# Performance work log

Measured on AMD Instinct MI355X. Metric: run time of the kernel, lower is better.

The kernel has to match this reference:

```python
import jax, jax.numpy as jnp
import numpy as np

N_EV, N_OBJ, D = 50000, 100000, 256
E1, E2 = 400000, 800000


def _ln(x, g, b):
    m = x.mean(-1, keepdims=True)
    v = x.var(-1, keepdims=True)
    return (x - m) * jax.lax.rsqrt(v + 1e-5) * g + b


def _lrelu(x):
    return jax.nn.leaky_relu(x, 0.2)


def setup_inputs():
    key = jax.random.key(0)
    ks = jax.random.split(key, 24)
    s = 1.0 / np.sqrt(D)
    W = lambda i, shp: (jax.random.normal(ks[i], shp, jnp.float32) * s)
    inp = {
        'object_X': jax.random.normal(ks[0], (N_OBJ, D), jnp.float32),
        'event_X': jax.random.normal(ks[1], (N_EV, D), jnp.float32),
        'Wo': W(2, (D, D)), 'bo': jnp.zeros((D,), jnp.float32),
        'go': jnp.ones((D,), jnp.float32), 'bon': jnp.zeros((D,), jnp.float32),
        'We': W(3, (D, D)), 'be': jnp.zeros((D,), jnp.float32),
        'ge': jnp.ones((D,), jnp.float32), 'ben': jnp.zeros((D,), jnp.float32),
        'Wu': W(4, (D, D)), 'bu': jnp.zeros((D,), jnp.float32),
        'Wl': W(5, (D, D)), 'bl': jnp.zeros((D,), jnp.float32),
        'g1': jnp.ones((D,), jnp.float32), 'b1': jnp.zeros((D,), jnp.float32),
        'g2': jnp.ones((D,), jnp.float32), 'b2': jnp.zeros((D,), jnp.float32),
        'Wh1': W(6, (D, D)), 'ah1': W(7, (2 * D,)),
        'Wh2': W(8, (D, D)), 'ah2': W(9, (2 * D,)),
        'oe_ev': jax.random.randint(ks[10], (E1,), 0, N_EV, jnp.int32),
        'oe_obj': jax.random.randint(ks[11], (E1,), 0, N_OBJ, jnp.int32),
        'hg_node': jax.random.randint(ks[12], (E2,), 0, N_EV + N_OBJ, jnp.int32),
        'hg_edge': jax.random.randint(ks[13], (E2,), 0, N_EV, jnp.int32),
        'total_events': N_EV,
    }
    return inp


def reference(object_X, event_X, Wo, bo, go, bon, We, be, ge, ben,
              Wu, bu, Wl, bl, g1, b1, g2, b2, Wh1, ah1, Wh2, ah2,
              oe_ev, oe_obj, hg_node, hg_edge, total_events):
    # proj chains (Dropout is identity at eval)
    obj = _ln(_lrelu(object_X @ Wo + bo), go, bon)
    ev = _ln(_lrelu(event_X @ We + be), ge, ben)
    # ObjectStateUpdater: aggregate incident-event features per object, project
    msg = jax.ops.segment_sum(ev[oe_ev], oe_obj, num_segments=N_OBJ)
    obj1 = _ln(_lrelu(msg @ Wu + bu) + obj, g1, b1)
    # LifecycleStateUpdater: linear lifecycle state transition
    obj2 = _ln(_lrelu(obj1 @ Wl + bl) + obj1, g2, b2)
    X = jnp.concatenate([ev, obj2], axis=0)  # [N_EV+N_OBJ, D]
    n_nodes = N_EV + N_OBJ

    def hgnn(X, W, a):
        m = (X @ W)[hg_node]  # [E2, D] gathered node messages
        cnt = jax.ops.segment_sum(jnp.ones((E2,), X.dtype), hg_edge, num_segments=total_events)
        ef = jax.ops.segment_sum(m, hg_edge, num_segments=total_events) / jnp.maximum(cnt, 1.0)[:, None]
        gth = ef[hg_edge]  # [E2, D] hyperedge feature per incidence
        score = _lrelu(m @ a[:D] + gth @ a[D:])  # [E2]
        smax = jax.ops.segment_max(score, hg_node, num_segments=n_nodes)
        e = jnp.exp(score - smax[hg_node])
        z = jax.ops.segment_sum(e, hg_node, num_segments=n_nodes)
        attn = e / jnp.maximum(z, 1e-9)[hg_node]
        out = jax.ops.segment_sum(attn[:, None] * gth, hg_node, num_segments=n_nodes)
        return _lrelu(out), attn

    h, _ = hgnn(X, Wh1, ah1)
    h, attn = hgnn(h, Wh2, ah2)  # layer-2 attention is what get_attention_weights() returns
    return (h, attn)
```

## Files before the change

### kernel.cpp

```cpp
#include <hip/hip_runtime.h>
#include <cstdio>

typedef __attribute__((ext_vector_type(8))) short short8_t;
typedef __attribute__((ext_vector_type(8))) unsigned short ushort8_t;
typedef __attribute__((ext_vector_type(4))) unsigned short us4;
typedef __attribute__((ext_vector_type(4))) float f32x4;

__device__ __forceinline__ unsigned short f2bf(float f) {
  unsigned u = __float_as_uint(f);
  u = u + 0x7FFFu + ((u >> 16) & 1u);
  return (unsigned short)(u >> 16);
}
__device__ __forceinline__ float bf2f(unsigned short h) {
  return __uint_as_float((unsigned)h << 16);
}
__device__ __forceinline__ float lrelu(float x) { return x > 0.f ? x : 0.2f * x; }


__global__ void k_transpose_w6(const float* __restrict__ W0, const float* __restrict__ W1,
                               const float* __restrict__ W2, const float* __restrict__ W3,
                               const float* __restrict__ W4, const float* __restrict__ W5,
                               unsigned short* __restrict__ WT) {
  int which = blockIdx.x >> 8, k = blockIdx.x & 255, n = threadIdx.x;
  const float* W = which == 0 ? W0 : which == 1 ? W1 : which == 2 ? W2
                 : which == 3 ? W3 : which == 4 ? W4 : W5;
  WT[(size_t)which * 65536 + n * 256 + k] = f2bf(W[k * 256 + n]);
}


__global__ void k_count3(const int* __restrict__ hg_node, const int* __restrict__ hg_edge,
                         const int* __restrict__ oe_obj, int* __restrict__ cn,
                         int* __restrict__ ce, int* __restrict__ co, int nE2, int nE1) {
  int e = blockIdx.x * blockDim.x + threadIdx.x;
  if (e < nE2) {
    atomicAdd(&cn[hg_node[e]], 1);
    atomicAdd(&ce[hg_edge[e]], 1);
  }
  if (e < nE1) atomicAdd(&co[oe_obj[e]], 1);
}

__global__ void k_fill3(const int* __restrict__ hg_node, const int* __restrict__ hg_edge,
                        const int* __restrict__ oe_ev, const int* __restrict__ oe_obj,
                        const int* __restrict__ NS, const int* __restrict__ ES,
                        const int* __restrict__ OS, int* __restrict__ curn,
                        int* __restrict__ cure, int* __restrict__ curo,
                        int2* __restrict__ PE, int* __restrict__ NDe, int* __restrict__ EVo,
                        int nE2, int nE1) {
  int e = blockIdx.x * blockDim.x + threadIdx.x;
  if (e < nE2) {
    int sn = hg_node[e], se = hg_edge[e];
    int pn = NS[sn] + atomicAdd(&curn[sn], 1);
    PE[pn] = make_int2(e, se);
    int pe = ES[se] + atomicAdd(&cure[se], 1);
    NDe[pe] = sn;
  }
  if (e < nE1) {
    int so = oe_obj[e];
    int po = OS[so] + atomicAdd(&curo[so], 1);
    EVo[po] = oe_ev[e];
  }
}

__global__ __launch_bounds__(1024) void k_scan3(const int* __restrict__ c0, int* __restrict__ s0,
                                                int n0, const int* __restrict__ c1,
                                                int* __restrict__ s1, int n1,
                                                const int* __restrict__ c2, int* __restrict__ s2,
                                                int n2) {
  const int* cnt;
  int* starts;
  int n;
  if (blockIdx.x == 0) { cnt = c0; starts = s0; n = n0; }
  else if (blockIdx.x == 1) { cnt = c1; starts = s1; n = n1; }
  else { cnt = c2; starts = s2; n = n2; }
  __shared__ int wsum[16];
  int tid = threadIdx.x, lane = tid & 63, w = tid >> 6;
  int carry = 0;
  for (int base = 0; base < n; base += 4096) {
    int i0 = base + tid * 4;
    int4 c = make_int4(0, 0, 0, 0);
    if (i0 + 3 < n) c = *(const int4*)(cnt + i0);
    else {
      if (i0 < n) c.x = cnt[i0];
      if (i0 + 1 < n) c.y = cnt[i0 + 1];
      if (i0 + 2 < n) c.z = cnt[i0 + 2];
      if (i0 + 3 < n) c.w = cnt[i0 + 3];
    }
    int tsum = c.x + c.y + c.z + c.w;
    int inc = tsum;
    for (int o = 1; o < 64; o <<= 1) {
      int v = __shfl_up(inc, o);
      if (lane >= o) inc += v;
    }
    if (lane == 63) wsum[w] = inc;
    __syncthreads();
    int woff = 0;
    for (int k = 0; k < w; k++) woff += wsum[k];
    int excl = carry + woff + inc - tsum;
    if (i0 < n) starts[i0] = excl;
    if (i0 + 1 < n) starts[i0 + 1] = excl + c.x;
    if (i0 + 2 < n) starts[i0 + 2] = excl + c.x + c.y;
    if (i0 + 3 < n) starts[i0 + 3] = excl + c.x + c.y + c.z;
    int total = 0;
    for (int k = 0; k < 16; k++) total += wsum[k];
    carry += total;
    __syncthreads();
  }
  if (tid == 0) starts[n] = carry;
}

template <int HAS_SKIP, int A_F32>
__global__ __launch_bounds__(256) void k_gemm_ln(const void* __restrict__ Av,
                                                 const unsigned short* __restrict__ Bt,
                                                 const float* __restrict__ bias,
                                                 const float* __restrict__ gamma,
                                                 const float* __restrict__ beta,
                                                 const unsigned short* skip,
                                                 unsigned short* outb, int rows) {
  __shared__ unsigned short As[64][40];
  __shared__ unsigned short Bs[256][40];
  int tid = threadIdx.x;
  int wave = tid >> 6, lane = tid & 63;
  int quad = lane >> 4, l16 = lane & 15;
  size_t row0 = (size_t)blockIdx.x * 64;

  f32x4 acc[16];
#pragma unroll
  for (int i = 0; i < 16; i++) acc[i] = (f32x4){0.f, 0.f, 0.f, 0.f};

  int ar = tid >> 2, ac = (tid & 3) * 8;
  size_t arow = row0 + ar;
  for (int k0 = 0; k0 < 256; k0 += 32) {
    if (A_F32) {
      float4 f0 = make_float4(0.f, 0.f, 0.f, 0.f), f1 = f0;
      if (arow < (size_t)rows) {
        const float4* ap = (const float4*)((const float*)Av + arow * 256 + k0 + ac);
        f0 = ap[0];
        f1 = ap[1];
      }
      us4 u0 = {f2bf(f0.x), f2bf(f0.y), f2bf(f0.z), f2bf(f0.w)};
      us4 u1 = {f2bf(f1.x), f2bf(f1.y), f2bf(f1.z), f2bf(f1.w)};
      *(us4*)&As[ar][ac] = u0;
      *(us4*)&As[ar][ac + 4] = u1;
    } else {
      *(ushort8_t*)&As[ar][ac] =
          *(const ushort8_t*)&((const unsigned short*)Av)[arow * 256 + k0 + ac];
    }
    const unsigned short* bp = &Bt[(size_t)tid * 256 + k0];
    *(ushort8_t*)&Bs[tid][0] = *(const ushort8_t*)&bp[0];
    *(ushort8_t*)&Bs[tid][8] = *(const ushort8_t*)&bp[8];
    *(ushort8_t*)&Bs[tid][16] = *(const ushort8_t*)&bp[16];
    *(ushort8_t*)&Bs[tid][24] = *(const ushort8_t*)&bp[24];
    __syncthreads();
    short8_t afrag = *(const short8_t*)&As[wave * 16 + l16][quad * 8];
#pragma unroll
    for (int nt = 0; nt < 16; nt++) {
      short8_t bfrag = *(const short8_t*)&Bs[nt * 16 + l16][quad * 8];
      acc[nt] = __builtin_amdgcn_mfma_f32_16x16x32_bf16(afrag, bfrag, acc[nt], 0, 0, 0);
    }
    __syncthreads();
  }

  size_t rbase = row0 + wave * 16 + quad * 4;
#pragma unroll
  for (int nt = 0; nt < 16; nt++) {
    int col = nt * 16 + l16;
    float bv = bias[col];
#pragma unroll
    for (int r = 0; r < 4; r++) {
      float x = lrelu(acc[nt][r] + bv);
      if (HAS_SKIP) {
        if (rbase + r < (size_t)rows) x += bf2f(skip[(rbase + r) * 256 + col]);
      }
      acc[nt][r] = x;
    }
  }
  float s[4] = {0, 0, 0, 0}, q[4] = {0, 0, 0, 0};
#pragma unroll
  for (int nt = 0; nt < 16; nt++)
#pragma unroll
    for (int r = 0; r < 4; r++) {
      float x = acc[nt][r];
      s[r] += x;
      q[r] += x * x;
    }
#pragma unroll
  for (int o = 1; o < 16; o <<= 1)
#pragma unroll
    for (int r = 0; r < 4; r++) {
      s[r] += __shfl_xor(s[r], o);
      q[r] += __shfl_xor(q[r], o);
    }
  float mr[4], rs[4];
#pragma unroll
  for (int r = 0; r < 4; r++) {
    float m = s[r] * (1.f / 256.f);
    float v = q[r] * (1.f / 256.f) - m * m;
    mr[r] = m;
    rs[r] = rsqrtf(v + 1e-5f);
  }
#pragma unroll
  for (int nt = 0; nt < 16; nt++) {
    int col = nt * 16 + l16;
    float g = gamma[col], bb = beta[col];
#pragma unroll
    for (int r = 0; r < 4; r++) {
      if (rbase + r < (size_t)rows) {
        float y = (acc[nt][r] - mr[r]) * rs[r] * g + bb;
        outb[(rbase + r) * 256 + col] = f2bf(y);
      }
    }
  }
}

__global__ __launch_bounds__(256) void k_gemm_xw(unsigned short* A,
                                                 const unsigned short* __restrict__ Bt,
                                                 const float* __restrict__ a1,
                                                 float* __restrict__ s1, int rows) {
  __shared__ unsigned short As[64][40];
  __shared__ unsigned short Bs[256][40];
  int tid = threadIdx.x;
  int wave = tid >> 6, lane = tid & 63;
  int quad = lane >> 4, l16 = lane & 15;
  size_t row0 = (size_t)blockIdx.x * 64;

  f32x4 acc[16];
#pragma unroll
  for (int i = 0; i < 16; i++) acc[i] = (f32x4){0.f, 0.f, 0.f, 0.f};

  int ar = tid >> 2, ac = (tid & 3) * 8;
  for (int k0 = 0; k0 < 256; k0 += 32) {
    *(ushort8_t*)&As[ar][ac] = *(const ushort8_t*)&A[(row0 + ar) * 256 + k0 + ac];
    const unsigned short* bp = &Bt[(size_t)tid * 256 + k0];
    *(ushort8_t*)&Bs[tid][0] = *(const ushort8_t*)&bp[0];
    *(ushort8_t*)&Bs[tid][8] = *(const ushort8_t*)&bp[8];
    *(ushort8_t*)&Bs[tid][16] = *(const ushort8_t*)&bp[16];
    *(ushort8_t*)&Bs[tid][24] = *(const ushort8_t*)&bp[24];
    __syncthreads();
    short8_t afrag = *(const short8_t*)&As[wave * 16 + l16][quad * 8];
#pragma unroll
    for (int nt = 0; nt < 16; nt++) {
      short8_t bfrag = *(const short8_t*)&Bs[nt * 16 + l16][quad * 8];
      acc[nt] = __builtin_amdgcn_mfma_f32_16x16x32_bf16(afrag, bfrag, acc[nt], 0, 0, 0);
    }
    __syncthreads();
  }

  size_t rbase = row0 + wave * 16 + quad * 4;
  float s[4] = {0, 0, 0, 0};
#pragma unroll
  for (int nt = 0; nt < 16; nt++) {
    float av = a1[nt * 16 + l16];
#pragma unroll
    for (int r = 0; r < 4; r++) s[r] += acc[nt][r] * av;
  }
#pragma unroll
  for (int o = 1; o < 16; o <<= 1)
#pragma unroll
    for (int r = 0; r < 4; r++) s[r] += __shfl_xor(s[r], o);
#pragma unroll
  for (int nt = 0; nt < 16; nt++) {
    int col = nt * 16 + l16;
#pragma unroll
    for (int r = 0; r < 4; r++)
      if (rbase + r < (size_t)rows) A[(rbase + r) * 256 + col] = f2bf(acc[nt][r]);
  }
  if (l16 == 0) {
#pragma unroll
    for (int r = 0; r < 4; r++)
      if (rbase + r < (size_t)rows) s1[rbase + r] = s[r];
  }
}


__global__ __launch_bounds__(256) void k_edge_gather(const unsigned short* __restrict__ XW,
                                                     const int* __restrict__ ES,
                                                     const int* __restrict__ NDe,
                                                     const float* __restrict__ a2,
                                                     unsigned short* __restrict__ EF,
                                                     float* __restrict__ s2, int nEdges) {
  int wave = threadIdx.x >> 6, lane = threadIdx.x & 63;
  int r = blockIdx.x * 4 + wave;
  if (r >= nEdges) return;
  int s = ES[r], e = ES[r + 1];
  int cnt = e - s;
  float4 acc = make_float4(0.f, 0.f, 0.f, 0.f);
  if (cnt <= 64) {
    int myn = 0;
    if (lane < cnt) myn = NDe[s + lane];
    for (int base = 0; base < cnt; base += 8) {
      us4 u[8];
      float f[8];
#pragma unroll
      for (int t = 0; t < 8; t++) {
        int j2 = base + t;
        int n1 = __shfl(myn, j2);
        u[t] = ((const us4*)(XW + (size_t)n1 * 256))[lane];
        f[t] = (j2 < cnt) ? 1.f : 0.f;
      }
#pragma unroll
      for (int t = 0; t < 8; t++) {
        acc.x += f[t] * bf2f(u[t].x);
        acc.y += f[t] * bf2f(u[t].y);
        acc.z += f[t] * bf2f(u[t].z);
        acc.w += f[t] * bf2f(u[t].w);
      }
    }
  } else {
    for (int j = s; j < e; j++) {
      int n = NDe[j];
      us4 u = ((const us4*)(XW + (size_t)n * 256))[lane];
      acc.x += bf2f(u.x); acc.y += bf2f(u.y);
      acc.z += bf2f(u.z); acc.w += bf2f(u.w);
    }
  }
  float inv = 1.f / (float)(cnt > 1 ? cnt : 1);
  acc.x *= inv; acc.y *= inv; acc.z *= inv; acc.w *= inv;
  us4 ub = {f2bf(acc.x), f2bf(acc.y), f2bf(acc.z), f2bf(acc.w)};
  ((us4*)(EF + (size_t)r * 256))[lane] = ub;
  float4 a = ((const float4*)a2)[lane];
  float d = acc.x * a.x + acc.y * a.y + acc.z * a.z + acc.w * a.w;
  for (int o = 32; o; o >>= 1) d += __shfl_xor(d, o);
  if (lane == 0) s2[r] = d;
}

template <int WRITE_ATTN>
__global__ __launch_bounds__(256) void k_node_gather(const int* __restrict__ NS,
                                                     const int2* __restrict__ PE,
                                                     const float* __restrict__ s1,
                                                     const float* __restrict__ s2,
                                                     const unsigned short* __restrict__ EF,
                                                     unsigned short* outb, float* outf,
                                                     float* attn_out, int nNodes) {
  int wave = threadIdx.x >> 6, lane = threadIdx.x & 63;
  int n = blockIdx.x * 4 + wave;
  if (n >= nNodes) return;
  int s = NS[n], e = NS[n + 1];
  int cnt = e - s;
  float s1n = s1[n];
  float4 acc = make_float4(0.f, 0.f, 0.f, 0.f);
  if (cnt <= 64) {
    int mye0 = 0, myed = 0;
    float myscore = -3.4e38f;
    bool act = lane < cnt;
    if (act) {
      int2 pe = PE[s + lane];
      mye0 = pe.x;
      myed = pe.y;
      myscore = lrelu(s1n + s2[myed]);
    }
    float mymax = myscore;
    for (int o = 32; o; o >>= 1) mymax = fmaxf(mymax, __shfl_xor(mymax, o));
    float myexp = act ? __expf(myscore - mymax) : 0.f;
    float mysum = myexp;
    for (int o = 32; o; o >>= 1) mysum += __shfl_xor(mysum, o);
    float zinv = 1.f / fmaxf(mysum, 1e-9f);
    float myw = myexp * zinv;
    if (WRITE_ATTN && act) attn_out[mye0] = myw;
    for (int base = 0; base < cnt; base += 8) {
      us4 v[8];
      float w[8];
#pragma unroll
      for (int t = 0; t < 8; t++) {
        int j2 = base + t;
        int ed = __shfl(myed, j2);
        w[t] = __shfl(myw, j2);
        v[t] = ((const us4*)(EF + (size_t)ed * 256))[lane];
      }
#pragma unroll
      for (int t = 0; t < 8; t++) {
        acc.x += w[t] * bf2f(v[t].x);
        acc.y += w[t] * bf2f(v[t].y);
        acc.z += w[t] * bf2f(v[t].z);
        acc.w += w[t] * bf2f(v[t].w);
      }
    }
  } else {
    float mymax = -3.4e38f;
    for (int j = s + lane; j < e; j += 64) {
      mymax = fmaxf(mymax, lrelu(s1n + s2[PE[j].y]));
    }
    for (int o = 32; o; o >>= 1) mymax = fmaxf(mymax, __shfl_xor(mymax, o));
    float mysum = 0.f;
    for (int j = s + lane; j < e; j += 64) {
      mysum += __expf(lrelu(s1n + s2[PE[j].y]) - mymax);
    }
    for (int o = 32; o; o >>= 1) mysum += __shfl_xor(mysum, o);
    float zinv = 1.f / fmaxf(mysum, 1e-9f);
    for (int j = s; j < e; j++) {
      int2 pe = PE[j];
      float w = __expf(lrelu(s1n + s2[pe.y]) - mymax) * zinv;
      if (WRITE_ATTN) {
        if (lane == 0) attn_out[pe.x] = w;
      }
      us4 v = ((const us4*)(EF + (size_t)pe.y * 256))[lane];
      acc.x += w * bf2f(v.x); acc.y += w * bf2f(v.y);
      acc.z += w * bf2f(v.z); acc.w += w * bf2f(v.w);
    }
  }
  acc.x = lrelu(acc.x); acc.y = lrelu(acc.y);
  acc.z = lrelu(acc.z); acc.w = lrelu(acc.w);
  if (outb) {
    us4 u = {f2bf(acc.x), f2bf(acc.y), f2bf(acc.z), f2bf(acc.w)};
    ((us4*)(outb + (size_t)n * 256))[lane] = u;
  } else {
    ((float4*)(outf + (size_t)n * 256))[lane] = acc;
  }
}

__global__ __launch_bounds__(256) void k_obj_gather(const unsigned short* __restrict__ EVB,
                                                    const int* __restrict__ OS,
                                                    const int* __restrict__ EVo,
                                                    unsigned short* __restrict__ outb,
                                                    int nObj) {
  int wave = threadIdx.x >> 6, lane = threadIdx.x & 63;
  int o = blockIdx.x * 4 + wave;
  if (o >= nObj) return;
  int s = OS[o], e = OS[o + 1];
  int cnt = e - s;
  float4 acc = make_float4(0.f, 0.f, 0.f, 0.f);
  if (cnt <= 64) {
    int myev = 0;
    if (lane < cnt) myev = EVo[s + lane];
    for (int base = 0; base < cnt; base += 8) {
      us4 u[8];
      float f[8];
#pragma unroll
      for (int t = 0; t < 8; t++) {
        int j2 = base + t;
        int v1 = __shfl(myev, j2);
        u[t] = ((const us4*)(EVB + (size_t)v1 * 256))[lane];
        f[t] = (j2 < cnt) ? 1.f : 0.f;
      }
#pragma unroll
      for (int t = 0; t < 8; t++) {
        acc.x += f[t] * bf2f(u[t].x);
        acc.y += f[t] * bf2f(u[t].y);
        acc.z += f[t] * bf2f(u[t].z);
        acc.w += f[t] * bf2f(u[t].w);
      }
    }
  } else {
    for (int j = s; j < e; j++) {
      int ev = EVo[j];
      us4 u = ((const us4*)(EVB + (size_t)ev * 256))[lane];
      acc.x += bf2f(u.x); acc.y += bf2f(u.y);
      acc.z += bf2f(u.z); acc.w += bf2f(u.w);
    }
  }
  us4 u = {f2bf(acc.x), f2bf(acc.y), f2bf(acc.z), f2bf(acc.w)};
  ((us4*)(outb + (size_t)o * 256))[lane] = u;
}


extern "C" void kernel_launch(void* const* d_in, const int* in_sizes, int n_in,
                              void* d_out, int out_size, void* d_ws, size_t ws_size,
                              hipStream_t stream) {
  (void)n_in; (void)out_size;
  const float* object_X = (const float*)d_in[0];
  const float* event_X = (const float*)d_in[1];
  const float* Wo = (const float*)d_in[2];   const float* bo = (const float*)d_in[3];
  const float* go = (const float*)d_in[4];   const float* bon = (const float*)d_in[5];
  const float* We = (const float*)d_in[6];   const float* be = (const float*)d_in[7];
  const float* ge = (const float*)d_in[8];   const float* ben = (const float*)d_in[9];
  const float* Wu = (const float*)d_in[10];  const float* bu = (const float*)d_in[11];
  const float* Wl = (const float*)d_in[12];  const float* bl = (const float*)d_in[13];
  const float* g1 = (const float*)d_in[14];  const float* b1 = (const float*)d_in[15];
  const float* g2 = (const float*)d_in[16];  const float* b2 = (const float*)d_in[17];
  const float* Wh1 = (const float*)d_in[18]; const float* ah1 = (const float*)d_in[19];
  const float* Wh2 = (const float*)d_in[20]; const float* ah2 = (const float*)d_in[21];
  const int* oe_ev = (const int*)d_in[22];
  const int* oe_obj = (const int*)d_in[23];
  const int* hg_node = (const int*)d_in[24];
  const int* hg_edge = (const int*)d_in[25];

  const int N_OBJ = in_sizes[0] / 256;
  const int N_EV = in_sizes[1] / 256;
  const int E1 = in_sizes[22];
  const int E2 = in_sizes[24];
  const int NN = N_EV + N_OBJ;
  const int MEV = ((N_EV + 63) / 64) * 64;
  const int MOB = ((N_OBJ + 63) / 64) * 64;
  const int MX = ((NN + 63) / 64) * 64;
  const int EMX = E2 > E1 ? E2 : E1;

  char* p = (char*)d_ws;
  auto take = [&](size_t bytes) {
    char* r = p;
    p += (bytes + 255) & ~(size_t)255;
    return r;
  };
  unsigned short* WT = (unsigned short*)take((size_t)6 * 65536 * 2);
  unsigned short* XBF = (unsigned short*)take((size_t)MX * 256 * 2);
  unsigned short* SB = (unsigned short*)take((size_t)MOB * 256 * 2);
  unsigned short* EF = SB;
  float* S1 = (float*)take((size_t)NN * 4);
  float* S2 = (float*)take((size_t)N_EV * 4);
  int* NS = (int*)take((size_t)(NN + 1) * 4);
  int* ES = (int*)take((size_t)(N_EV + 1) * 4);
  int* OS = (int*)take((size_t)(N_OBJ + 1) * 4);
  int* CNTn = (int*)take((size_t)NN * 4);
  int* CNTe = (int*)take((size_t)N_EV * 4);
  int* CNTo = (int*)take((size_t)N_OBJ * 4);
  int2* PEn = (int2*)take((size_t)E2 * 8);
  int* NDe = (int*)take((size_t)E2 * 4);
  int* EVo = (int*)take((size_t)E1 * 4);
  size_t need = (size_t)(p - (char*)d_ws);
  if (need > ws_size)
    fprintf(stderr, "[kernel_launch] WS OVERFLOW: need=%zu have=%zu\n", need, ws_size);

  float* out = (float*)d_out;
  unsigned short* OBJB = (unsigned short*)d_out;

  k_transpose_w6<<<6 * 256, 256, 0, stream>>>(We, Wo, Wu, Wl, Wh1, Wh2, WT);

  if (MX > NN)
    hipMemsetAsync(XBF + (size_t)NN * 256, 0, (size_t)(MX - NN) * 512, stream);

  size_t cnt_span = (size_t)((char*)PEn - (char*)CNTn);
  hipMemsetAsync(CNTn, 0, cnt_span, stream);
  k_count3<<<(EMX + 255) / 256, 256, 0, stream>>>(hg_node, hg_edge, oe_obj, CNTn, CNTe, CNTo,
                                                  E2, E1);
  k_scan3<<<3, 1024, 0, stream>>>(CNTn, NS, NN, CNTe, ES, N_EV, CNTo, OS, N_OBJ);
  hipMemsetAsync(CNTn, 0, cnt_span, stream);
  k_fill3<<<(EMX + 255) / 256, 256, 0, stream>>>(hg_node, hg_edge, oe_ev, oe_obj, NS, ES, OS,
                                                 CNTn, CNTe, CNTo, PEn, NDe, EVo, E2, E1);

  k_gemm_ln<0, 1><<<MEV / 64, 256, 0, stream>>>(event_X, WT + 0 * 65536, be, ge, ben, nullptr,
                                                XBF, N_EV);
  k_gemm_ln<0, 1><<<MOB / 64, 256, 0, stream>>>(object_X, WT + 1 * 65536, bo, go, bon, nullptr,
                                                OBJB, N_OBJ);
  k_obj_gather<<<(N_OBJ + 3) / 4, 256, 0, stream>>>(XBF, OS, EVo, SB, N_OBJ);
  k_gemm_ln<1, 0><<<MOB / 64, 256, 0, stream>>>(SB, WT + 2 * 65536, bu, g1, b1, OBJB, SB,
                                                N_OBJ);
  k_gemm_ln<1, 0><<<MOB / 64, 256, 0, stream>>>(SB, WT + 3 * 65536, bl, g2, b2, SB,
                                                XBF + (size_t)N_EV * 256, N_OBJ);

  k_gemm_xw<<<MX / 64, 256, 0, stream>>>(XBF, WT + 4 * 65536, ah1, S1, NN);
  k_edge_gather<<<(N_EV + 3) / 4, 256, 0, stream>>>(XBF, ES, NDe, ah1 + 256, EF, S2, N_EV);
  k_node_gather<0><<<(NN + 3) / 4, 256, 0, stream>>>(NS, PEn, S1, S2, EF, XBF, nullptr,
                                                     nullptr, NN);
  k_gemm_xw<<<MX / 64, 256, 0, stream>>>(XBF, WT + 5 * 65536, ah2, S1, NN);
  k_edge_gather<<<(N_EV + 3) / 4, 256, 0, stream>>>(XBF, ES, NDe, ah2 + 256, EF, S2, N_EV);
  k_node_gather<1><<<(NN + 3) / 4, 256, 0, stream>>>(NS, PEn, S1, S2, EF, nullptr, out,
                                                     out + (size_t)NN * 256, NN);
}
```

Before: 1.433 ms.

## Keep full packed weight in LDS with persistent strip-looping GEMM blocks

Weights are pre-packed into MFMA fragment order so each GEMM block loads the whole 256x256 bf16 weight (128 KB) into LDS once. Persistent blocks (grid 256) then loop over 64-row strips, with A fragments loaded straight from global memory into registers, and the per-k-step syncthreads and LDS staging of A are removed. This cuts repeated weight reloads and barriers. The cost is very high LDS use per block, which limits occupancy to one block per CU, and no overlap of A loads with MFMA work.

```diff
diff --git a/kernel.cpp b/kernel.cpp
--- a/kernel.cpp
+++ b/kernel.cpp
@@ -16,15 +16,17 @@
 }
 __device__ __forceinline__ float lrelu(float x) { return x > 0.f ? x : 0.2f * x; }
 
-
-__global__ void k_transpose_w6(const float* __restrict__ W0, const float* __restrict__ W1,
-                               const float* __restrict__ W2, const float* __restrict__ W3,
-                               const float* __restrict__ W4, const float* __restrict__ W5,
-                               unsigned short* __restrict__ WT) {
+__global__ void k_pack_w6(const float* __restrict__ W0, const float* __restrict__ W1,
+                          const float* __restrict__ W2, const float* __restrict__ W3,
+                          const float* __restrict__ W4, const float* __restrict__ W5,
+                          unsigned short* __restrict__ WF) {
   int which = blockIdx.x >> 8, k = blockIdx.x & 255, n = threadIdx.x;
   const float* W = which == 0 ? W0 : which == 1 ? W1 : which == 2 ? W2
                  : which == 3 ? W3 : which == 4 ? W4 : W5;
-  WT[(size_t)which * 65536 + n * 256 + k] = f2bf(W[k * 256 + n]);
+  int nt = n >> 4, l16 = n & 15;
+  int ks = k >> 5, quad = (k >> 3) & 3, j = k & 7;
+  size_t idx = ((size_t)which << 16) + (size_t)(((nt * 8 + ks) * 64 + quad * 16 + l16) * 8 + j);
+  WF[idx] = f2bf(W[k * 256 + n]);
 }
 
 
@@ -110,164 +112,168 @@
 
 template <int HAS_SKIP, int A_F32>
 __global__ __launch_bounds__(256) void k_gemm_ln(const void* __restrict__ Av,
-                                                 const unsigned short* __restrict__ Bt,
+                                                 const unsigned short* __restrict__ WF,
                                                  const float* __restrict__ bias,
                                                  const float* __restrict__ gamma,
                                                  const float* __restrict__ beta,
                                                  const unsigned short* skip,
-                                                 unsigned short* outb, int rows) {
-  __shared__ unsigned short As[64][40];
-  __shared__ unsigned short Bs[256][40];
+                                                 unsigned short* outb, int rows, int nStrips) {
+  __shared__ unsigned short Bs[65536];
   int tid = threadIdx.x;
+#pragma unroll
+  for (int i = 0; i < 32; i++)
+    *(ushort8_t*)&Bs[(i * 256 + tid) * 8] = *(const ushort8_t*)&WF[(size_t)(i * 256 + tid) * 8];
+  __syncthreads();
   int wave = tid >> 6, lane = tid & 63;
   int quad = lane >> 4, l16 = lane & 15;
-  size_t row0 = (size_t)blockIdx.x * 64;
-
-  f32x4 acc[16];
-#pragma unroll
-  for (int i = 0; i < 16; i++) acc[i] = (f32x4){0.f, 0.f, 0.f, 0.f};
-
-  int ar = tid >> 2, ac = (tid & 3) * 8;
-  size_t arow = row0 + ar;
-  for (int k0 = 0; k0 < 256; k0 += 32) {
+
+  for (int strip = blockIdx.x; strip < nStrips; strip += gridDim.x) {
+    size_t row0 = (size_t)strip * 64 + wave * 16;
+    size_t arow = row0 + l16;
+    short8_t af[8];
     if (A_F32) {
-      float4 f0 = make_float4(0.f, 0.f, 0.f, 0.f), f1 = f0;
-      if (arow < (size_t)rows) {
-        const float4* ap = (const float4*)((const float*)Av + arow * 256 + k0 + ac);
-        f0 = ap[0];
-        f1 = ap[1];
-      }
-      us4 u0 = {f2bf(f0.x), f2bf(f0.y), f2bf(f0.z), f2bf(f0.w)};
-      us4 u1 = {f2bf(f1.x), f2bf(f1.y), f2bf(f1.z), f2bf(f1.w)};
-      *(us4*)&As[ar][ac] = u0;
-      *(us4*)&As[ar][ac + 4] = u1;
+      bool inr = arow < (size_t)rows;
+      const float4* ap = (const float4*)((const float*)Av + arow * 256);
+#pragma unroll
+      for (int ks = 0; ks < 8; ks++) {
+        float4 f0 = make_float4(0.f, 0.f, 0.f, 0.f), f1 = f0;
+        if (inr) {
+          f0 = ap[ks * 8 + quad * 2];
+          f1 = ap[ks * 8 + quad * 2 + 1];
+        }
+        ushort8_t a;
+        a[0] = f2bf(f0.x); a[1] = f2bf(f0.y); a[2] = f2bf(f0.z); a[3] = f2bf(f0.w);
+        a[4] = f2bf(f1.x); a[5] = f2bf(f1.y); a[6] = f2bf(f1.z); a[7] = f2bf(f1.w);
+        af[ks] = (short8_t)a;
+      }
     } else {
-      *(ushort8_t*)&As[ar][ac] =
-          *(const ushort8_t*)&((const unsigned short*)Av)[arow * 256 + k0 + ac];
-    }
-    const unsigned short* bp = &Bt[(size_t)tid * 256 + k0];
-    *(ushort8_t*)&Bs[tid][0] = *(const ushort8_t*)&bp[0];
-    *(ushort8_t*)&Bs[tid][8] = *(const ushort8_t*)&bp[8];
-    *(ushort8_t*)&Bs[tid][16] = *(const ushort8_t*)&bp[16];
-    *(ushort8_t*)&Bs[tid][24] = *(const ushort8_t*)&bp[24];
-    __syncthreads();
-    short8_t afrag = *(const short8_t*)&As[wave * 16 + l16][quad * 8];
+      const ushort8_t* ap = (const ushort8_t*)((const unsigned short*)Av + arow * 256);
+#pragma unroll
+      for (int ks = 0; ks < 8; ks++) af[ks] = (short8_t)ap[ks * 4 + quad];
+    }
+
+    f32x4 acc[16];
+#pragma unroll
+    for (int i = 0; i < 16; i++) acc[i] = (f32x4){0.f, 0.f, 0.f, 0.f};
+#pragma unroll
+    for (int ks = 0; ks < 8; ks++) {
+#pragma unroll
+      for (int nt = 0; nt < 16; nt++) {
+        short8_t bf = *(const short8_t*)&Bs[((nt * 8 + ks) * 64 + lane) * 8];
+        acc[nt] = __builtin_amdgcn_mfma_f32_16x16x32_bf16(af[ks], bf, acc[nt], 0, 0, 0);
+      }
+    }
+
+    size_t rbase = row0 + quad * 4;
 #pragma unroll
     for (int nt = 0; nt < 16; nt++) {
-      short8_t bfrag = *(const short8_t*)&Bs[nt * 16 + l16][quad * 8];
-      acc[nt] = __builtin_amdgcn_mfma_f32_16x16x32_bf16(afrag, bfrag, acc[nt], 0, 0, 0);
-    }
-    __syncthreads();
-  }
-
-  size_t rbase = row0 + wave * 16 + quad * 4;
-#pragma unroll
-  for (int nt = 0; nt < 16; nt++) {
-    int col = nt * 16 + l16;
-    float bv = bias[col];
+      int col = nt * 16 + l16;
+      float bv = bias[col];
+#pragma unroll
+      for (int r = 0; r < 4; r++) {
+        float x = lrelu(acc[nt][r] + bv);
+        if (HAS_SKIP) {
+          if (rbase + r < (size_t)rows) x += bf2f(skip[(rbase + r) * 256 + col]);
+        }
+        acc[nt][r] = x;
+      }
+    }
+    float s[4] = {0, 0, 0, 0}, q[4] = {0, 0, 0, 0};
+#pragma unroll
+    for (int nt = 0; nt < 16; nt++)
+#pragma unroll
+      for (int r = 0; r < 4; r++) {
+        float x = acc[nt][r];
+        s[r] += x;
+        q[r] += x * x;
+      }
+#pragma unroll
+    for (int o = 1; o < 16; o <<= 1)
+#pragma unroll
+      for (int r = 0; r < 4; r++) {
+        s[r] += __shfl_xor(s[r], o);
+        q[r] += __shfl_xor(q[r], o);
+      }
+    float mr[4], rs[4];
 #pragma unroll
     for (int r = 0; r < 4; r++) {
-      float x = lrelu(acc[nt][r] + bv);
-      if (HAS_SKIP) {
-        if (rbase + r < (size_t)rows) x += bf2f(skip[(rbase + r) * 256 + col]);
-      }
-      acc[nt][r] = x;
-    }
-  }
-  float s[4] = {0, 0, 0, 0}, q[4] = {0, 0, 0, 0};
-#pragma unroll
-  for (int nt = 0; nt < 16; nt++)
-#pragma unroll
-    for (int r = 0; r < 4; r++) {
-      float x = acc[nt][r];
-      s[r] += x;
-      q[r] += x * x;
-    }
-#pragma unroll
-  for (int o = 1; o < 16; o <<= 1)
-#pragma unroll
-    for (int r = 0; r < 4; r++) {
-      s[r] += __shfl_xor(s[r], o);
-      q[r] += __shfl_xor(q[r], o);
-    }
-  float mr[4], rs[4];
-#pragma unroll
-  for (int r = 0; r < 4; r++) {
-    float m = s[r] * (1.f / 256.f);
-    float v = q[r] * (1.f / 256.f) - m * m;
-    mr[r] = m;
-    rs[r] = rsqrtf(v + 1e-5f);
-  }
-#pragma unroll
-  for (int nt = 0; nt < 16; nt++) {
-    int col = nt * 16 + l16;
-    float g = gamma[col], bb = beta[col];
-#pragma unroll
-    for (int r = 0; r < 4; r++) {
-      if (rbase + r < (size_t)rows) {
-        float y = (acc[nt][r] - mr[r]) * rs[r] * g + bb;
-        outb[(rbase + r) * 256 + col] = f2bf(y);
+      float m = s[r] * (1.f / 256.f);
+      float v = q[r] * (1.f / 256.f) - m * m;
+      mr[r] = m;
+      rs[r] = rsqrtf(v + 1e-5f);
+    }
+#pragma unroll
+    for (int nt = 0; nt < 16; nt++) {
+      int col = nt * 16 + l16;
+      float g = gamma[col], bb = beta[col];
+#pragma unroll
+      for (int r = 0; r < 4; r++) {
+        if (rbase + r < (size_t)rows) {
+          float y = (acc[nt][r] - mr[r]) * rs[r] * g + bb;
+          outb[(rbase + r) * 256 + col] = f2bf(y);
+        }
       }
     }
   }
 }
 
 __global__ __launch_bounds__(256) void k_gemm_xw(unsigned short* A,
-                                                 const unsigned short* __restrict__ Bt,
+                                                 const unsigned short* __restrict__ WF,
                                                  const float* __restrict__ a1,
-                                                 float* __restrict__ s1, int rows) {
-  __shared__ unsigned short As[64][40];
-  __shared__ unsigned short Bs[256][40];
+                                                 float* __restrict__ s1, int rows, int nStrips) {
+  __shared__ unsigned short Bs[65536];
   int tid = threadIdx.x;
+#pragma unroll
+  for (int i = 0; i < 32; i++)
+    *(ushort8_t*)&Bs[(i * 256 + tid) * 8] = *(const ushort8_t*)&WF[(size_t)(i * 256 + tid) * 8];
+  __syncthreads();
   int wave = tid >> 6, lane = tid & 63;
   int quad = lane >> 4, l16 = lane & 15;
-  size_t row0 = (size_t)blockIdx.x * 64;
-
-  f32x4 acc[16];
-#pragma unroll
-  for (int i = 0; i < 16; i++) acc[i] = (f32x4){0.f, 0.f, 0.f, 0.f};
-
-  int ar = tid >> 2, ac = (tid & 3) * 8;
-  for (int k0 = 0; k0 < 256; k0 += 32) {
-    *(ushort8_t*)&As[ar][ac] = *(const ushort8_t*)&A[(row0 + ar) * 256 + k0 + ac];
-    const unsigned short* bp = &Bt[(size_t)tid * 256 + k0];
-    *(ushort8_t*)&Bs[tid][0] = *(const ushort8_t*)&bp[0];
-    *(ushort8_t*)&Bs[tid][8] = *(const ushort8_t*)&bp[8];
-    *(ushort8_t*)&Bs[tid][16] = *(const ushort8_t*)&bp[16];
-    *(ushort8_t*)&Bs[tid][24] = *(const ushort8_t*)&bp[24];
-    __syncthreads();
-    short8_t afrag = *(const short8_t*)&As[wave * 16 + l16][quad * 8];
+
+  for (int strip = blockIdx.x; strip < nStrips; strip += gridDim.x) {
+    size_t row0 = (size_t)strip * 64 + wave * 16;
+    size_t arow = row0 + l16;
+    short8_t af[8];
+    const ushort8_t* ap = (const ushort8_t*)(A + arow * 256);
+#pragma unroll
+    for (int ks = 0; ks < 8; ks++) af[ks] = (short8_t)ap[ks * 4 + quad];
+
+    f32x4 acc[16];
+#pragma unroll
+    for (int i = 0; i < 16; i++) acc[i] = (f32x4){0.f, 0.f, 0.f, 0.f};
+#pragma unroll
+    for (int ks = 0; ks < 8; ks++) {
+#pragma unroll
+      for (int nt = 0; nt < 16; nt++) {
+        short8_t bf = *(const short8_t*)&Bs[((nt * 8 + ks) * 64 + lane) * 8];
+        acc[nt] = __builtin_amdgcn_mfma_f32_16x16x32_bf16(af[ks], bf, acc[nt], 0, 0, 0);
+      }
+    }
+
+    size_t rbase = row0 + quad * 4;
+    float s[4] = {0, 0, 0, 0};
 #pragma unroll
     for (int nt = 0; nt < 16; nt++) {
-      short8_t bfrag = *(const short8_t*)&Bs[nt * 16 + l16][quad * 8];
-      acc[nt] = __builtin_amdgcn_mfma_f32_16x16x32_bf16(afrag, bfrag, acc[nt], 0, 0, 0);
-    }
-    __syncthreads();
-  }
-
-  size_t rbase = row0 + wave * 16 + quad * 4;
-  float s[4] = {0, 0, 0, 0};
-#pragma unroll
-  for (int nt = 0; nt < 16; nt++) {
-    float av = a1[nt * 16 + l16];
-#pragma unroll
-    for (int r = 0; r < 4; r++) s[r] += acc[nt][r] * av;
-  }
-#pragma unroll
-  for (int o = 1; o < 16; o <<= 1)
-#pragma unroll
-    for (int r = 0; r < 4; r++) s[r] += __shfl_xor(s[r], o);
-#pragma unroll
-  for (int nt = 0; nt < 16; nt++) {
-    int col = nt * 16 + l16;
-#pragma unroll
-    for (int r = 0; r < 4; r++)
-      if (rbase + r < (size_t)rows) A[(rbase + r) * 256 + col] = f2bf(acc[nt][r]);
-  }
-  if (l16 == 0) {
-#pragma unroll
-    for (int r = 0; r < 4; r++)
-      if (rbase + r < (size_t)rows) s1[rbase + r] = s[r];
+      float av = a1[nt * 16 + l16];
+#pragma unroll
+      for (int r = 0; r < 4; r++) s[r] += acc[nt][r] * av;
+    }
+#pragma unroll
+    for (int o = 1; o < 16; o <<= 1)
+#pragma unroll
+      for (int r = 0; r < 4; r++) s[r] += __shfl_xor(s[r], o);
+#pragma unroll
+    for (int nt = 0; nt < 16; nt++) {
+      int col = nt * 16 + l16;
+#pragma unroll
+      for (int r = 0; r < 4; r++)
+        if (rbase + r < (size_t)rows) A[(rbase + r) * 256 + col] = f2bf(acc[nt][r]);
+    }
+    if (l16 == 0) {
+#pragma unroll
+      for (int r = 0; r < 4; r++)
+        if (rbase + r < (size_t)rows) s1[rbase + r] = s[r];
+    }
   }
 }
 
@@ -489,7 +495,7 @@
     p += (bytes + 255) & ~(size_t)255;
     return r;
   };
-  unsigned short* WT = (unsigned short*)take((size_t)6 * 65536 * 2);
+  unsigned short* WF = (unsigned short*)take((size_t)6 * 65536 * 2);
   unsigned short* XBF = (unsigned short*)take((size_t)MX * 256 * 2);
   unsigned short* SB = (unsigned short*)take((size_t)MOB * 256 * 2);
   unsigned short* EF = SB;
@@ -511,7 +517,7 @@
   float* out = (float*)d_out;
   unsigned short* OBJB = (unsigned short*)d_out;
 
-  k_transpose_w6<<<6 * 256, 256, 0, stream>>>(We, Wo, Wu, Wl, Wh1, Wh2, WT);
+  k_pack_w6<<<6 * 256, 256, 0, stream>>>(We, Wo, Wu, Wl, Wh1, Wh2, WF);
 
   if (MX > NN)
     hipMemsetAsync(XBF + (size_t)NN * 256, 0, (size_t)(MX - NN) * 512, stream);
@@ -525,21 +531,21 @@
   k_fill3<<<(EMX + 255) / 256, 256, 0, stream>>>(hg_node, hg_edge, oe_ev, oe_obj, NS, ES, OS,
                                                  CNTn, CNTe, CNTo, PEn, NDe, EVo, E2, E1);
 
-  k_gemm_ln<0, 1><<<MEV / 64, 256, 0, stream>>>(event_X, WT + 0 * 65536, be, ge, ben, nullptr,
-                                                XBF, N_EV);
-  k_gemm_ln<0, 1><<<MOB / 64, 256, 0, stream>>>(object_X, WT + 1 * 65536, bo, go, bon, nullptr,
-                                                OBJB, N_OBJ);
+  k_gemm_ln<0, 1><<<256, 256, 0, stream>>>(event_X, WF + 0 * 65536, be, ge, ben, nullptr,
+                                           XBF, N_EV, MEV / 64);
+  k_gemm_ln<0, 1><<<256, 256, 0, stream>>>(object_X, WF + 1 * 65536, bo, go, bon, nullptr,
+                                           OBJB, N_OBJ, MOB / 64);
   k_obj_gather<<<(N_OBJ + 3) / 4, 256, 0, stream>>>(XBF, OS, EVo, SB, N_OBJ);
-  k_gemm_ln<1, 0><<<MOB / 64, 256, 0, stream>>>(SB, WT + 2 * 65536, bu, g1, b1, OBJB, SB,
-                                                N_OBJ);
-  k_gemm_ln<1, 0><<<MOB / 64, 256, 0, stream>>>(SB, WT + 3 * 65536, bl, g2, b2, SB,
-                                                XBF + (size_t)N_EV * 256, N_OBJ);
-
-  k_gemm_xw<<<MX / 64, 256, 0, stream>>>(XBF, WT + 4 * 65536, ah1, S1, NN);
+  k_gemm_ln<1, 0><<<256, 256, 0, stream>>>(SB, WF + 2 * 65536, bu, g1, b1, OBJB, SB, N_OBJ,
+                                           MOB / 64);
+  k_gemm_ln<1, 0><<<256, 256, 0, stream>>>(SB, WF + 3 * 65536, bl, g2, b2, SB,
+                                           XBF + (size_t)N_EV * 256, N_OBJ, MOB / 64);
+
+  k_gemm_xw<<<256, 256, 0, stream>>>(XBF, WF + 4 * 65536, ah1, S1, NN, MX / 64);
   k_edge_gather<<<(N_EV + 3) / 4, 256, 0, stream>>>(XBF, ES, NDe, ah1 + 256, EF, S2, N_EV);
   k_node_gather<0><<<(NN + 3) / 4, 256, 0, stream>>>(NS, PEn, S1, S2, EF, XBF, nullptr,
                                                      nullptr, NN);
-  k_gemm_xw<<<MX / 64, 256, 0, stream>>>(XBF, WT + 5 * 65536, ah2, S1, NN);
+  k_gemm_xw<<<256, 256, 0, stream>>>(XBF, WF + 5 * 65536, ah2, S1, NN, MX / 64);
   k_edge_gather<<<(N_EV + 3) / 4, 256, 0, stream>>>(XBF, ES, NDe, ah2 + 256, EF, S2, N_EV);
   k_node_gather<1><<<(NN + 3) / 4, 256, 0, stream>>>(NS, PEn, S1, S2, EF, nullptr, out,
                                                      out + (size_t)NN * 256, NN);
```

Result: slower. 2.050 ms (+43.0%).
